# Performance work log

Measured on AMD Instinct MI355X. Metric: run time of the kernel, lower is better.

Reference implementation:

```python
import jax, jax.numpy as jnp
import numpy as np

N = 100_000      # nodes
E = 1_600_000    # edges
F_IN = 128       # n_features == conv_dim1..3
F_OUT = 256      # concat_dim
G = 2000         # number of graphs in the batch
EPS = 1e-5       # BatchNorm eps


def _xavier(k, shape):
    fan_in, fan_out = shape[-2], shape[-1]
    lim = float(np.sqrt(6.0 / (fan_in + fan_out)))
    return jax.random.uniform(k, shape, jnp.float32, -lim, lim)


def setup_inputs() -> dict:
    key = jax.random.key(0)
    ks = jax.random.split(key, 8)
    x = jax.random.normal(ks[0], (N, F_IN), jnp.float32)
    edge_index = jax.random.randint(ks[1], (2, E), 0, N, dtype=jnp.int64)
    batch = jnp.sort(jax.random.randint(ks[2], (N,), 0, G, dtype=jnp.int64))
    # layers 1..5: F_IN -> F_IN (stacked), layer 6: F_IN -> F_OUT
    Wi = _xavier(ks[3], (5, F_IN, F_IN))   # ARMA init_weight per layer
    Wr = _xavier(ks[4], (5, F_IN, F_IN))   # ARMA root_weight per layer
    b = jnp.zeros((5, F_IN), jnp.float32)  # ARMA bias per layer
    g = jnp.ones((5, F_IN), jnp.float32)   # BN gamma
    be = jnp.zeros((5, F_IN), jnp.float32) # BN beta
    Wi6 = _xavier(ks[5], (F_IN, F_OUT))
    Wr6 = _xavier(ks[6], (F_IN, F_OUT))
    b6 = jnp.zeros((F_OUT,), jnp.float32)
    g6 = jnp.ones((F_OUT,), jnp.float32)
    be6 = jnp.zeros((F_OUT,), jnp.float32)
    return dict(x=x, edge_index=edge_index, batch=batch, Wi=Wi, Wr=Wr, b=b,
                g=g, be=be, Wi6=Wi6, Wr6=Wr6, b6=b6, g6=g6, be6=be6)


def _arma(x, norm, row, col, Wi_l, Wr_l, b_l):
    # ARMAConv (num_stacks=1, num_layers=1, act=ReLU):
    #   out = ReLU( A_norm @ (x W_init) + x W_root + b )
    h = x @ Wi_l                                           # [N, F_out]
    msg = h[row] * norm[:, None]                           # gather + scale, [E, F_out]
    agg = jax.ops.segment_sum(msg, col, num_segments=N)    # scatter-add
    return jax.nn.relu(agg + x @ Wr_l + b_l)


def _bn(x, gamma, beta):
    # BatchNorm1d, training mode (biased batch variance)
    mu = x.mean(axis=0)
    var = x.var(axis=0)
    return gamma * (x - mu) * jax.lax.rsqrt(var + EPS) + beta


def reference(x, edge_index, batch, Wi, Wr, b, g, be, Wi6, Wr6, b6, g6, be6):
    row, col = edge_index[0], edge_index[1]
    # gcn_norm without self loops: D^-1/2 A D^-1/2 edge weights
    deg = jax.ops.segment_sum(jnp.ones((E,), x.dtype), col, num_segments=N)
    dinv = jnp.where(deg > 0, jax.lax.rsqrt(deg), 0.0)
    norm = dinv[row] * dinv[col]                           # [E]

    h = x
    for l in range(5):  # fixed small layer count
        h = _arma(h, norm, row, col, Wi[l], Wr[l], b[l])   # outer F.relu is idempotent
        h = _bn(h, g[l], be[l])
    h = _arma(h, norm, row, col, Wi6, Wr6, b6)
    h = _bn(h, g6, be6)
    # global_add_pool over graph ids; dropout = identity (deterministic baseline)
    out = jax.ops.segment_sum(h, batch, num_segments=G)    # [G, F_OUT]
    return out
```

## Files before the change

kernel.cpp:

```cpp
#include <hip/hip_runtime.h>

#define Nn 100000
#define NP 100001
#define Ee 1600000
#define Gg 2000
#define EPSf 1e-5f

typedef unsigned short ushort_t;
typedef __attribute__((ext_vector_type(8))) short short8;
typedef __attribute__((ext_vector_type(4))) float f32x4;
typedef __attribute__((ext_vector_type(4))) unsigned u32x4;

__device__ inline float bf2f(unsigned int u) {
    union { unsigned int i; float f; } v; v.i = u << 16; return v.f;
}
__device__ inline unsigned short f2bf(float f) {
    unsigned int x = __float_as_uint(f);
    unsigned int r = (x + 0x7fffu + ((x >> 16) & 1u)) >> 16;
    return (unsigned short)r;
}
__device__ inline int ldidx(const void* a, int i, int i64) {
    return i64 ? (int)((const long long*)a)[i] : ((const int*)a)[i];
}
__device__ inline float ldflt(const void* p, long long i, int f32) {
    return f32 ? ((const float*)p)[i] : bf2f(((const ushort_t*)p)[i]);
}


__global__ void k_flags(const void* gones, const void* ei, int* flags) {
    if (threadIdx.x == 0 && blockIdx.x == 0) {
        unsigned w = *(const unsigned*)gones;
        flags[0] = (w == 0x3F800000u) ? 1 : 0;
        const int* e = (const int*)ei;
        int nz = 0;
        for (int i = 0; i < 256; i++) nz |= e[2 * i + 1];
        flags[1] = nz ? 0 : 1;
    }
}


__global__ void k_hist(const void* __restrict__ ei, int* __restrict__ deg, const int* __restrict__ flags) {
    int i = blockIdx.x * 256 + threadIdx.x;
    if (i < Ee) {
        int c = ldidx(ei, Ee + i, flags[1]);
        atomicAdd(&deg[c], 1);
    }
}

__global__ void k_dinv(const int* __restrict__ deg, float* __restrict__ dinv) {
    int i = blockIdx.x * 256 + threadIdx.x;
    if (i < Nn) { int d = deg[i]; dinv[i] = d > 0 ? rsqrtf((float)d) : 0.f; }
}

__global__ void k_scan1(const int* __restrict__ deg, int* __restrict__ off, int* __restrict__ part) {
    __shared__ int sh[1024];
    int i = blockIdx.x * 1024 + threadIdx.x;
    int v = (i < Nn) ? ((deg[i] + 3) & ~3) : 0;
    sh[threadIdx.x] = v;
    __syncthreads();
    for (int ofs = 1; ofs < 1024; ofs <<= 1) {
        int t = 0;
        if ((int)threadIdx.x >= ofs) t = sh[threadIdx.x - ofs];
        __syncthreads();
        sh[threadIdx.x] += t;
        __syncthreads();
    }
    if (i < Nn) off[i] = sh[threadIdx.x] - v;
    if (threadIdx.x == 1023) part[blockIdx.x] = sh[1023];
}

__global__ void k_scan2(int* part, int nb) {
    if (threadIdx.x == 0 && blockIdx.x == 0) {
        int run = 0;
        for (int i = 0; i < nb; i++) { int t = part[i]; part[i] = run; run += t; }
        part[nb] = run;
    }
}

__global__ void k_scan3(int* __restrict__ off, const int* __restrict__ part, int* __restrict__ cursor) {
    int i = blockIdx.x * 256 + threadIdx.x;
    if (i < Nn) {
        int v = off[i] + part[i >> 10];
        off[i] = v;
        cursor[i] = v;
    }
    if (i == 0) off[Nn] = part[98];
}

__global__ void k_fillp(const void* __restrict__ ei, int* __restrict__ cursor,
                        int* __restrict__ srcS, const int* __restrict__ flags) {
    int range = blockIdx.x & 7;
    int e = (blockIdx.x >> 3) * 256 + threadIdx.x;
    if (e < Ee) {
        int i64 = flags[1];
        int c = ldidx(ei, Ee + e, i64);
        if (c >= range * 12500 && c < (range + 1) * 12500) {
            int r = ldidx(ei, e, i64);
            int p = atomicAdd(&cursor[c], 1);
            srcS[p] = r;
        }
    }
}

__global__ void k_pad(const int* __restrict__ cursor, const int* __restrict__ off,
                      int* __restrict__ srcS) {
    int i = blockIdx.x * 256 + threadIdx.x;
    if (i < Nn) {
        int e = off[i + 1];
        for (int p = cursor[i]; p < e; p++) srcS[p] = Nn;
    }
}

__global__ void k_zrow(ushort_t* __restrict__ Hi) {
    int t = threadIdx.x;
    int fc = t >> 4, j = t & 15;
    Hi[((size_t)fc * NP + Nn) * 16 + j] = 0;
}

__global__ void k_cvtp(const void* b, const void* b6, const void* g, const void* g6,
                       const void* be, const void* be6,
                       float* __restrict__ biasF, float* __restrict__ gF,
                       float* __restrict__ beF, const int* __restrict__ flags) {
    int i = blockIdx.x * 256 + threadIdx.x;
    if (i >= 2688) return;
    int grp = i / 896, r = i - grp * 896;
    int f32 = flags[0];
    const void* srcs[6] = { b, b6, g, g6, be, be6 };
    float* dsts[3] = { biasF, gF, beF };
    const void* s = (r < 640) ? srcs[grp * 2] : srcs[grp * 2 + 1];
    int idx = (r < 640) ? r : r - 640;
    dsts[grp][r] = ldflt(s, idx, f32);
}

__global__ void k_cvtx(const void* __restrict__ x, ushort_t* __restrict__ xq, const int* __restrict__ flags) {
    int node = blockIdx.x * 256 + threadIdx.x;
    int fc = blockIdx.y;
    if (node < Nn) {
        union { ushort_t u[16]; u32x4 v[2]; } t;
        if (flags[0]) {
            const float* p = (const float*)x + (size_t)node * 128 + fc * 16;
#pragma unroll
            for (int j = 0; j < 16; j++) t.u[j] = f2bf(p[j]);
        } else {
            const ushort_t* p = (const ushort_t*)x + (size_t)node * 128 + fc * 16;
#pragma unroll
            for (int j = 0; j < 16; j++) t.u[j] = p[j];
        }
        u32x4* d = (u32x4*)(xq + ((size_t)fc * Nn + node) * 16);
        d[0] = t.v[0]; d[1] = t.v[1];
    }
}

__global__ void k_pack(const void* __restrict__ Wi, const void* __restrict__ Wr,
                       const void* __restrict__ Wi6, const void* __restrict__ Wr6,
                       ushort_t* __restrict__ Bp, const int* __restrict__ flags) {
    int idx = blockIdx.x * 256 + threadIdx.x;
    if (idx >= 229376) return;
    int f32 = flags[0];
    if (idx < 163840) {
        int l = idx / 32768, rem = idx - l * 32768;
        int kg = rem / 2048, rem2 = rem - kg * 2048;
        int n = rem2 / 8, j = rem2 - n * 8;
        int k = kg * 8 + j;
        float v = (n < 128) ? ldflt(Wi, (l * 128 + k) * 128 + n, f32)
                            : ldflt(Wr, (l * 128 + k) * 128 + (n - 128), f32);
        Bp[idx] = f2bf(v);
    } else {
        int idx2 = idx - 163840;
        int kg = idx2 / 4096, rem2 = idx2 - kg * 4096;
        int n = rem2 / 8, j = rem2 - n * 8;
        int k = kg * 8 + j;
        float v = (n < 256) ? ldflt(Wi6, k * 256 + n, f32) : ldflt(Wr6, k * 256 + (n - 256), f32);
        Bp[idx] = f2bf(v);
    }
}

__global__ void k_fold(const ushort_t* __restrict__ Bp, const float* __restrict__ stat,
                       const float* __restrict__ gamma, const float* __restrict__ beta,
                       const float* __restrict__ bias,
                       ushort_t* __restrict__ Bp2, float* __restrict__ hcorr, int ncat) {
    __shared__ float red[128];
    int n = blockIdx.x, k = threadIdx.x;
    int fhalf = ncat >> 1;
    float mu = stat[k] * (1.f / Nn);
    float var = stat[128 + k] * (1.f / Nn) - mu * mu;
    float rs = rsqrtf(var + EPSf);
    float s = gamma[k] * rs;
    float h = beta[k] - s * mu;
    size_t idx = ((size_t)(k >> 3) * ncat + n) * 8 + (k & 7);
    float w = bf2f(Bp[idx]);
    Bp2[idx] = f2bf(w * s);
    red[k] = h * w;
    __syncthreads();
    for (int m = 64; m > 0; m >>= 1) { if (k < m) red[k] += red[k + m]; __syncthreads(); }
    if (k == 0) hcorr[n] = red[0] + (n >= fhalf ? bias[n - fhalf] : 0.f);
}

__global__ void k_h0(const float* __restrict__ bias, float* __restrict__ hc, int ncat) {
    int n = blockIdx.x * 256 + threadIdx.x;
    if (n < ncat) hc[n] = n >= (ncat >> 1) ? bias[n - (ncat >> 1)] : 0.f;
}


__global__ __launch_bounds__(256) void k_gemm(
        const ushort_t* __restrict__ Aq,
        const ushort_t* __restrict__ Bp, const float* __restrict__ hcorr,
        const float* __restrict__ dinv,
        ushort_t* __restrict__ Hi, ushort_t* __restrict__ yq, int ncat) {
    __shared__ ushort_t stage[32 * 264];
    const int tid = threadIdx.x, lane = tid & 63, wid = tid >> 6;
    const int q = lane >> 4, l15 = lane & 15;
    const int fhalf = ncat >> 1;
    const int colW = blockIdx.y * 256 + wid * 64;

    short8 bfr[4][4];
    float hc[4];
#pragma unroll
    for (int kk = 0; kk < 4; kk++) {
        int kg = kk * 4 + q;
#pragma unroll
        for (int ct = 0; ct < 4; ct++)
            bfr[kk][ct] = *(const short8*)(Bp + ((size_t)kg * ncat + colW + ct * 16 + l15) * 8);
    }
#pragma unroll
    for (int ct = 0; ct < 4; ct++) hc[ct] = hcorr[colW + ct * 16 + l15];

    for (int t = 0; t < 4; t++) {
        int row0 = (blockIdx.x * 4 + t) * 64;
        if (row0 >= Nn) break;

        f32x4 acc[4][4];
        f32x4 z; z.x = 0.f; z.y = 0.f; z.z = 0.f; z.w = 0.f;
#pragma unroll
        for (int rt = 0; rt < 4; rt++)
#pragma unroll
            for (int ct = 0; ct < 4; ct++) acc[rt][ct] = z;

#pragma unroll
        for (int kk = 0; kk < 4; kk++) {
            int kg = kk * 4 + q;
            const ushort_t* ap = Aq + (size_t)(kg >> 1) * Nn * 16 + (kg & 1) * 8;
            short8 af[4];
#pragma unroll
            for (int rt = 0; rt < 4; rt++) {
                int node = row0 + rt * 16 + l15;
                if (node >= Nn) node = Nn - 1;
                af[rt] = *(const short8*)(ap + (size_t)node * 16);
            }
#pragma unroll
            for (int rt = 0; rt < 4; rt++)
#pragma unroll
                for (int ct = 0; ct < 4; ct++)
                    acc[rt][ct] = __builtin_amdgcn_mfma_f32_16x16x32_bf16(af[rt], bfr[kk][ct], acc[rt][ct], 0, 0, 0);
        }

#pragma unroll
        for (int half = 0; half < 2; half++) {
            __syncthreads();
#pragma unroll
            for (int ct = 0; ct < 4; ct++) {
                int lcol = wid * 64 + ct * 16 + l15;
                bool isHi = (blockIdx.y * 256 + lcol) < fhalf;
#pragma unroll
                for (int rt2 = 0; rt2 < 2; rt2++) {
                    int rt = half * 2 + rt2;
#pragma unroll
                    for (int r = 0; r < 4; r++) {
                        int grow = row0 + rt * 16 + q * 4 + r;
                        int gr = grow < Nn ? grow : 0;
                        float v = acc[rt][ct][r] + hc[ct];
                        if (isHi) v *= dinv[gr];
                        stage[(rt2 * 16 + q * 4 + r) * 264 + lcol] = f2bf(v);
                    }
                }
            }
            __syncthreads();
            for (int chunk = tid; chunk < 512; chunk += 256) {
                int cg = chunk & 15, rl = chunk >> 4;
                int node = row0 + half * 32 + rl;
                if (node < Nn) {
                    int gc0 = blockIdx.y * 256 + cg * 16;
                    const u32x4* sp = (const u32x4*)&stage[rl * 264 + cg * 16];
                    u32x4 v0 = sp[0], v1 = sp[1];
                    ushort_t* dst = (gc0 < fhalf)
                        ? Hi + ((size_t)(gc0 >> 4) * NP + node) * 16
                        : yq + ((size_t)((gc0 - fhalf) >> 4) * Nn + node) * 16;
                    u32x4* dp = (u32x4*)dst;
                    dp[0] = v0; dp[1] = v1;
                }
            }
        }
    }
}


__global__ __launch_bounds__(256) void k_agg8(const int* __restrict__ off, const int* __restrict__ src,
                                              const float* __restrict__ dinv, const unsigned* __restrict__ Hi2,
                                              unsigned* __restrict__ yq, float* __restrict__ stat,
                                              int F, int fcbase) {
    const int tid = threadIdx.x;
    const int w = tid >> 6, lane = tid & 63;
    const int sub = lane >> 3, fl = lane & 7;
    const int fc = fcbase + (blockIdx.x & 7);
    const int T = blockIdx.x >> 3;
    const unsigned* __restrict__ base = Hi2 + (size_t)fc * (NP * 8) + fl;
    float st0 = 0.f, st1 = 0.f, st2 = 0.f, st3 = 0.f;

#pragma unroll
    for (int pass = 0; pass < 4; pass++) {
        int node = T * 128 + pass * 32 + w * 8 + sub;
        bool valid = node < Nn;
        int p0 = 0, p1 = 0;
        if (valid) { p0 = off[node]; p1 = off[node + 1]; }
        float a0 = 0.f, a1 = 0.f;
        int p = p0;
        for (; p + 15 < p1; p += 16) {
            int4 sa = *(const int4*)(src + p);
            int4 sb = *(const int4*)(src + p + 4);
            int4 sc = *(const int4*)(src + p + 8);
            int4 sd = *(const int4*)(src + p + 12);
            unsigned u0 = base[(unsigned)sa.x * 8u];
            unsigned u1 = base[(unsigned)sa.y * 8u];
            unsigned u2 = base[(unsigned)sa.z * 8u];
            unsigned u3 = base[(unsigned)sa.w * 8u];
            unsigned u4 = base[(unsigned)sb.x * 8u];
            unsigned u5 = base[(unsigned)sb.y * 8u];
            unsigned u6 = base[(unsigned)sb.z * 8u];
            unsigned u7 = base[(unsigned)sb.w * 8u];
            unsigned u8 = base[(unsigned)sc.x * 8u];
            unsigned u9 = base[(unsigned)sc.y * 8u];
            unsigned uA = base[(unsigned)sc.z * 8u];
            unsigned uB = base[(unsigned)sc.w * 8u];
            unsigned uC = base[(unsigned)sd.x * 8u];
            unsigned uD = base[(unsigned)sd.y * 8u];
            unsigned uE = base[(unsigned)sd.z * 8u];
            unsigned uF = base[(unsigned)sd.w * 8u];
            a0 += bf2f(u0 & 0xffffu); a1 += bf2f(u0 >> 16);
            a0 += bf2f(u1 & 0xffffu); a1 += bf2f(u1 >> 16);
            a0 += bf2f(u2 & 0xffffu); a1 += bf2f(u2 >> 16);
            a0 += bf2f(u3 & 0xffffu); a1 += bf2f(u3 >> 16);
            a0 += bf2f(u4 & 0xffffu); a1 += bf2f(u4 >> 16);
            a0 += bf2f(u5 & 0xffffu); a1 += bf2f(u5 >> 16);
            a0 += bf2f(u6 & 0xffffu); a1 += bf2f(u6 >> 16);
            a0 += bf2f(u7 & 0xffffu); a1 += bf2f(u7 >> 16);
            a0 += bf2f(u8 & 0xffffu); a1 += bf2f(u8 >> 16);
            a0 += bf2f(u9 & 0xffffu); a1 += bf2f(u9 >> 16);
            a0 += bf2f(uA & 0xffffu); a1 += bf2f(uA >> 16);
            a0 += bf2f(uB & 0xffffu); a1 += bf2f(uB >> 16);
            a0 += bf2f(uC & 0xffffu); a1 += bf2f(uC >> 16);
            a0 += bf2f(uD & 0xffffu); a1 += bf2f(uD >> 16);
            a0 += bf2f(uE & 0xffffu); a1 += bf2f(uE >> 16);
            a0 += bf2f(uF & 0xffffu); a1 += bf2f(uF >> 16);
        }
        for (; p + 7 < p1; p += 8) {
            int4 sa = *(const int4*)(src + p);
            int4 sb = *(const int4*)(src + p + 4);
            unsigned u0 = base[(unsigned)sa.x * 8u];
            unsigned u1 = base[(unsigned)sa.y * 8u];
            unsigned u2 = base[(unsigned)sa.z * 8u];
            unsigned u3 = base[(unsigned)sa.w * 8u];
            unsigned u4 = base[(unsigned)sb.x * 8u];
            unsigned u5 = base[(unsigned)sb.y * 8u];
            unsigned u6 = base[(unsigned)sb.z * 8u];
            unsigned u7 = base[(unsigned)sb.w * 8u];
            a0 += bf2f(u0 & 0xffffu); a1 += bf2f(u0 >> 16);
            a0 += bf2f(u1 & 0xffffu); a1 += bf2f(u1 >> 16);
            a0 += bf2f(u2 & 0xffffu); a1 += bf2f(u2 >> 16);
            a0 += bf2f(u3 & 0xffffu); a1 += bf2f(u3 >> 16);
            a0 += bf2f(u4 & 0xffffu); a1 += bf2f(u4 >> 16);
            a0 += bf2f(u5 & 0xffffu); a1 += bf2f(u5 >> 16);
            a0 += bf2f(u6 & 0xffffu); a1 += bf2f(u6 >> 16);
            a0 += bf2f(u7 & 0xffffu); a1 += bf2f(u7 >> 16);
        }
        if (p < p1) {
            int4 sa = *(const int4*)(src + p);
            unsigned u0 = base[(unsigned)sa.x * 8u];
            unsigned u1 = base[(unsigned)sa.y * 8u];
            unsigned u2 = base[(unsigned)sa.z * 8u];
            unsigned u3 = base[(unsigned)sa.w * 8u];
            a0 += bf2f(u0 & 0xffffu); a1 += bf2f(u0 >> 16);
            a0 += bf2f(u1 & 0xffffu); a1 += bf2f(u1 >> 16);
            a0 += bf2f(u2 & 0xffffu); a1 += bf2f(u2 >> 16);
            a0 += bf2f(u3 & 0xffffu); a1 += bf2f(u3 >> 16);
        }
        if (valid) {
            float dv = dinv[node];
            unsigned* yp = yq + ((size_t)fc * Nn + node) * 8 + fl;
            unsigned uv = *yp;
            float vx = fmaxf(bf2f(uv & 0xffffu) + dv * a0, 0.f);
            float vy = fmaxf(bf2f(uv >> 16) + dv * a1, 0.f);
            *yp = (unsigned)f2bf(vx) | ((unsigned)f2bf(vy) << 16);
            st0 += vx; st1 += vx * vx;
            st2 += vy; st3 += vy * vy;
        }
    }
#pragma unroll
    for (int m = 8; m <= 32; m <<= 1) {
        st0 += __shfl_xor(st0, m, 64);
        st1 += __shfl_xor(st1, m, 64);
        st2 += __shfl_xor(st2, m, 64);
        st3 += __shfl_xor(st3, m, 64);
    }
    __shared__ float red[4][8][4];
    if (sub == 0) {
        red[w][fl][0] = st0; red[w][fl][1] = st1;
        red[w][fl][2] = st2; red[w][fl][3] = st3;
    }
    __syncthreads();
    if (tid < 32) {
        int rfl = tid >> 2, k = tid & 3;
        float s = red[0][rfl][k] + red[1][rfl][k] + red[2][rfl][k] + red[3][rfl][k];
        int f = fc * 16 + rfl * 2 + (k >> 1);
        atomicAdd(&stat[(k & 1) * F + f], s);
    }
}


__device__ inline int lb(const void* a, int n, int key, int i64) {
    int lo = 0, hi = n;
    while (lo < hi) { int mid = (lo + hi) >> 1; if (ldidx(a, mid, i64) < key) lo = mid + 1; else hi = mid; }
    return lo;
}

__global__ void k_pool(const ushort_t* __restrict__ y6q, const float* __restrict__ stat,
                       const float* __restrict__ g6, const float* __restrict__ be6,
                       const void* __restrict__ batch, void* __restrict__ out,
                       const int* __restrict__ flags) {
    int g = blockIdx.x;
    int f = threadIdx.x;
    int i64 = flags[1];
    int start = lb(batch, Nn, g, i64);
    int end = lb(batch, Nn, g + 1, i64);
    const ushort_t* yp = y6q + (size_t)(f >> 4) * Nn * 16 + (f & 15);
    float s = 0.f;
    for (int n = start; n < end; n++) s += bf2f(yp[(size_t)n * 16]);
    int cnt = end - start;
    float mu = stat[f] * (1.f / Nn);
    float var = stat[256 + f] * (1.f / Nn) - mu * mu;
    float rs = rsqrtf(var + EPSf);
    float val = g6[f] * rs * (s - (float)cnt * mu) + (float)cnt * be6[f];
    if (flags[0]) ((float*)out)[(size_t)g * 256 + f] = val;
    else          ((ushort_t*)out)[(size_t)g * 256 + f] = f2bf(val);
}


extern "C" void kernel_launch(void* const* d_in, const int* in_sizes, int n_in,
                              void* d_out, int out_size, void* d_ws, size_t ws_size,
                              hipStream_t stream) {
    const void* x    = d_in[0];
    const void* ei   = d_in[1];
    const void* batch= d_in[2];
    const void* Wi   = d_in[3];
    const void* Wr   = d_in[4];
    const void* b    = d_in[5];
    const void* g    = d_in[6];
    const void* be   = d_in[7];
    const void* Wi6  = d_in[8];
    const void* Wr6  = d_in[9];
    const void* b6   = d_in[10];
    const void* g6   = d_in[11];
    const void* be6  = d_in[12];

    char* p = (char*)d_ws;
    auto alloc = [&](size_t bytes) { char* r = p; p += (bytes + 511) & ~(size_t)511; return r; };
    ushort_t* HiB  = (ushort_t*)alloc((size_t)NP * 256 * 2);
    ushort_t* xq   = (ushort_t*)alloc((size_t)Nn * 128 * 2);
    ushort_t* yAq  = (ushort_t*)alloc((size_t)Nn * 128 * 2);
    ushort_t* yBq  = (ushort_t*)alloc((size_t)Nn * 128 * 2);
    ushort_t* y6q  = (ushort_t*)alloc((size_t)Nn * 256 * 2);
    int* srcS      = (int*)alloc(((size_t)Ee + 4 * Nn + 64) * 4);
    int* off       = (int*)alloc((size_t)(Nn + 1) * 4);
    int* cursor    = (int*)alloc((size_t)Nn * 4);
    int* deg       = (int*)alloc((size_t)Nn * 4);
    float* dinv    = (float*)alloc((size_t)Nn * 4);
    int* part      = (int*)alloc(128 * 4);
    float* statsA  = (float*)alloc(6 * 512 * 4);
    ushort_t* Bp   = (ushort_t*)alloc(229376 * 2);
    ushort_t* Bp2  = (ushort_t*)alloc(65536 * 2);
    float* hcorrA  = (float*)alloc(512 * 4);
    int* flags     = (int*)alloc(2 * 4);
    float* biasF   = (float*)alloc(896 * 4);
    float* gF      = (float*)alloc(896 * 4);
    float* beF     = (float*)alloc(896 * 4);
    const unsigned* Hi2 = (const unsigned*)HiB;

    const int AGG_GRID = 782 * 8;
    const int GEMM_GRID = 391;

    k_flags<<<1, 64, 0, stream>>>(g, ei, flags);
    k_cvtp<<<11, 256, 0, stream>>>(b, b6, g, g6, be, be6, biasF, gF, beF, flags);

    hipMemsetAsync(deg, 0, (size_t)Nn * 4, stream);
    hipMemsetAsync(statsA, 0, 6 * 512 * 4, stream);
    k_hist<<<6250, 256, 0, stream>>>(ei, deg, flags);
    k_dinv<<<391, 256, 0, stream>>>(deg, dinv);
    k_scan1<<<98, 1024, 0, stream>>>(deg, off, part);
    k_scan2<<<1, 64, 0, stream>>>(part, 98);
    k_scan3<<<391, 256, 0, stream>>>(off, part, cursor);
    k_fillp<<<50000, 256, 0, stream>>>(ei, cursor, srcS, flags);
    k_pad<<<391, 256, 0, stream>>>(cursor, off, srcS);
    k_zrow<<<1, 256, 0, stream>>>(HiB);
    k_pack<<<896, 256, 0, stream>>>(Wi, Wr, Wi6, Wr6, Bp, flags);
    k_cvtx<<<dim3(391, 8), 256, 0, stream>>>(x, xq, flags);
    k_h0<<<1, 256, 0, stream>>>(biasF, hcorrA, 256);

    k_gemm<<<dim3(GEMM_GRID, 1), 256, 0, stream>>>(xq, Bp, hcorrA, dinv, HiB, yAq, 256);
    k_agg8<<<AGG_GRID, 256, 0, stream>>>(off, srcS, dinv, Hi2, (unsigned*)yAq, statsA, 128, 0);
    k_fold<<<256, 128, 0, stream>>>(Bp + 32768, statsA, gF, beF, biasF + 128, Bp2, hcorrA, 256);

    k_gemm<<<dim3(GEMM_GRID, 1), 256, 0, stream>>>(yAq, Bp2, hcorrA, dinv, HiB, yBq, 256);
    k_agg8<<<AGG_GRID, 256, 0, stream>>>(off, srcS, dinv, Hi2, (unsigned*)yBq, statsA + 512, 128, 0);
    k_fold<<<256, 128, 0, stream>>>(Bp + 65536, statsA + 512, gF + 128, beF + 128, biasF + 256, Bp2, hcorrA, 256);

    k_gemm<<<dim3(GEMM_GRID, 1), 256, 0, stream>>>(yBq, Bp2, hcorrA, dinv, HiB, yAq, 256);
    k_agg8<<<AGG_GRID, 256, 0, stream>>>(off, srcS, dinv, Hi2, (unsigned*)yAq, statsA + 1024, 128, 0);
    k_fold<<<256, 128, 0, stream>>>(Bp + 98304, statsA + 1024, gF + 256, beF + 256, biasF + 384, Bp2, hcorrA, 256);

    k_gemm<<<dim3(GEMM_GRID, 1), 256, 0, stream>>>(yAq, Bp2, hcorrA, dinv, HiB, yBq, 256);
    k_agg8<<<AGG_GRID, 256, 0, stream>>>(off, srcS, dinv, Hi2, (unsigned*)yBq, statsA + 1536, 128, 0);
    k_fold<<<256, 128, 0, stream>>>(Bp + 131072, statsA + 1536, gF + 384, beF + 384, biasF + 512, Bp2, hcorrA, 256);

    k_gemm<<<dim3(GEMM_GRID, 1), 256, 0, stream>>>(yBq, Bp2, hcorrA, dinv, HiB, yAq, 256);
    k_agg8<<<AGG_GRID, 256, 0, stream>>>(off, srcS, dinv, Hi2, (unsigned*)yAq, statsA + 2048, 128, 0);
    k_fold<<<512, 128, 0, stream>>>(Bp + 163840, statsA + 2048, gF + 512, beF + 512, biasF + 640, Bp2, hcorrA, 512);

    k_gemm<<<dim3(GEMM_GRID, 2), 256, 0, stream>>>(yAq, Bp2, hcorrA, dinv, HiB, y6q, 512);
    k_agg8<<<AGG_GRID, 256, 0, stream>>>(off, srcS, dinv, Hi2, (unsigned*)y6q, statsA + 2560, 256, 0);
    k_agg8<<<AGG_GRID, 256, 0, stream>>>(off, srcS, dinv, Hi2, (unsigned*)y6q, statsA + 2560, 256, 8);
    k_pool<<<Gg, 256, 0, stream>>>(y6q, statsA + 2560, gF + 640, beF + 640, batch, d_out, flags);
}
```

Before: 1.244 ms.

## Sort nodes by degree bucket for aggregation and shrink GEMM tiles per block

Adds a counting sort of nodes into degree buckets (histogram, prefix, scatter) so the aggregation kernel processes nodes of similar degree together through a permutation, reducing lane divergence and load imbalance within waves. The GEMM kernel now processes one 64-row tile per block instead of four, with a correspondingly larger grid, to increase parallelism. The cost is three extra setup kernels, an extra indirection per node in aggregation that scatters the output writes, and the loss of per-block reuse of loaded B fragments across tiles.

```diff
diff --git a/kernel.cpp b/kernel.cpp
--- a/kernel.cpp
+++ b/kernel.cpp
@@ -115,6 +115,31 @@
     int t = threadIdx.x;
     int fc = t >> 4, j = t & 15;
     Hi[((size_t)fc * NP + Nn) * 16 + j] = 0;
+}
+
+
+__global__ void k_bh(const int* __restrict__ deg, int* __restrict__ bh) {
+    int i = blockIdx.x * 256 + threadIdx.x;
+    if (i < Nn) {
+        int b = (deg[i] + 3) >> 2; if (b > 255) b = 255;
+        atomicAdd(&bh[b], 1);
+    }
+}
+
+__global__ void k_bp(const int* __restrict__ bh, int* __restrict__ bc) {
+    if (threadIdx.x == 0 && blockIdx.x == 0) {
+        int run = 0;
+        for (int i = 0; i < 256; i++) { bc[i] = run; run += bh[i]; }
+    }
+}
+
+__global__ void k_bs(const int* __restrict__ deg, int* __restrict__ bc, int* __restrict__ perm) {
+    int i = blockIdx.x * 256 + threadIdx.x;
+    if (i < Nn) {
+        int b = (deg[i] + 3) >> 2; if (b > 255) b = 255;
+        int p = atomicAdd(&bc[b], 1);
+        perm[p] = i;
+    }
 }
 
 __global__ void k_cvtp(const void* b, const void* b6, const void* g, const void* g6,
@@ -212,6 +237,7 @@
     const int q = lane >> 4, l15 = lane & 15;
     const int fhalf = ncat >> 1;
     const int colW = blockIdx.y * 256 + wid * 64;
+    const int row0 = blockIdx.x * 64;
 
     short8 bfr[4][4];
     float hc[4];
@@ -225,69 +251,64 @@
 #pragma unroll
     for (int ct = 0; ct < 4; ct++) hc[ct] = hcorr[colW + ct * 16 + l15];
 
-    for (int t = 0; t < 4; t++) {
-        int row0 = (blockIdx.x * 4 + t) * 64;
-        if (row0 >= Nn) break;
-
-        f32x4 acc[4][4];
-        f32x4 z; z.x = 0.f; z.y = 0.f; z.z = 0.f; z.w = 0.f;
+    f32x4 acc[4][4];
+    f32x4 z; z.x = 0.f; z.y = 0.f; z.z = 0.f; z.w = 0.f;
+#pragma unroll
+    for (int rt = 0; rt < 4; rt++)
+#pragma unroll
+        for (int ct = 0; ct < 4; ct++) acc[rt][ct] = z;
+
+#pragma unroll
+    for (int kk = 0; kk < 4; kk++) {
+        int kg = kk * 4 + q;
+        const ushort_t* ap = Aq + (size_t)(kg >> 1) * Nn * 16 + (kg & 1) * 8;
+        short8 af[4];
+#pragma unroll
+        for (int rt = 0; rt < 4; rt++) {
+            int node = row0 + rt * 16 + l15;
+            if (node >= Nn) node = Nn - 1;
+            af[rt] = *(const short8*)(ap + (size_t)node * 16);
+        }
 #pragma unroll
         for (int rt = 0; rt < 4; rt++)
 #pragma unroll
-            for (int ct = 0; ct < 4; ct++) acc[rt][ct] = z;
-
-#pragma unroll
-        for (int kk = 0; kk < 4; kk++) {
-            int kg = kk * 4 + q;
-            const ushort_t* ap = Aq + (size_t)(kg >> 1) * Nn * 16 + (kg & 1) * 8;
-            short8 af[4];
-#pragma unroll
-            for (int rt = 0; rt < 4; rt++) {
-                int node = row0 + rt * 16 + l15;
-                if (node >= Nn) node = Nn - 1;
-                af[rt] = *(const short8*)(ap + (size_t)node * 16);
-            }
-#pragma unroll
-            for (int rt = 0; rt < 4; rt++)
-#pragma unroll
-                for (int ct = 0; ct < 4; ct++)
-                    acc[rt][ct] = __builtin_amdgcn_mfma_f32_16x16x32_bf16(af[rt], bfr[kk][ct], acc[rt][ct], 0, 0, 0);
-        }
-
-#pragma unroll
-        for (int half = 0; half < 2; half++) {
-            __syncthreads();
-#pragma unroll
-            for (int ct = 0; ct < 4; ct++) {
-                int lcol = wid * 64 + ct * 16 + l15;
-                bool isHi = (blockIdx.y * 256 + lcol) < fhalf;
-#pragma unroll
-                for (int rt2 = 0; rt2 < 2; rt2++) {
-                    int rt = half * 2 + rt2;
-#pragma unroll
-                    for (int r = 0; r < 4; r++) {
-                        int grow = row0 + rt * 16 + q * 4 + r;
-                        int gr = grow < Nn ? grow : 0;
-                        float v = acc[rt][ct][r] + hc[ct];
-                        if (isHi) v *= dinv[gr];
-                        stage[(rt2 * 16 + q * 4 + r) * 264 + lcol] = f2bf(v);
-                    }
+            for (int ct = 0; ct < 4; ct++)
+                acc[rt][ct] = __builtin_amdgcn_mfma_f32_16x16x32_bf16(af[rt], bfr[kk][ct], acc[rt][ct], 0, 0, 0);
+    }
+
+#pragma unroll
+    for (int half = 0; half < 2; half++) {
+        __syncthreads();
+#pragma unroll
+        for (int ct = 0; ct < 4; ct++) {
+            int lcol = wid * 64 + ct * 16 + l15;
+            bool isHi = (blockIdx.y * 256 + lcol) < fhalf;
+#pragma unroll
+            for (int rt2 = 0; rt2 < 2; rt2++) {
+                int rt = half * 2 + rt2;
+#pragma unroll
+                for (int r = 0; r < 4; r++) {
+                    int grow = row0 + rt * 16 + q * 4 + r;
+                    int gr = grow < Nn ? grow : 0;
+                    float v = acc[rt][ct][r] + hc[ct];
+                    if (isHi) v *= dinv[gr];
+                    stage[(rt2 * 16 + q * 4 + r) * 264 + lcol] = f2bf(v);
                 }
             }
-            __syncthreads();
-            for (int chunk = tid; chunk < 512; chunk += 256) {
-                int cg = chunk & 15, rl = chunk >> 4;
-                int node = row0 + half * 32 + rl;
-                if (node < Nn) {
-                    int gc0 = blockIdx.y * 256 + cg * 16;
-                    const u32x4* sp = (const u32x4*)&stage[rl * 264 + cg * 16];
-                    u32x4 v0 = sp[0], v1 = sp[1];
-                    ushort_t* dst = (gc0 < fhalf)
-                        ? Hi + ((size_t)(gc0 >> 4) * NP + node) * 16
-                        : yq + ((size_t)((gc0 - fhalf) >> 4) * Nn + node) * 16;
-                    u32x4* dp = (u32x4*)dst;
-                    dp[0] = v0; dp[1] = v1;
-                }
+        }
+        __syncthreads();
+        for (int chunk = tid; chunk < 512; chunk += 256) {
+            int cg = chunk & 15, rl = chunk >> 4;
+            int node = row0 + half * 32 + rl;
+            if (node < Nn) {
+                int gc0 = blockIdx.y * 256 + cg * 16;
+                const u32x4* sp = (const u32x4*)&stage[rl * 264 + cg * 16];
+                u32x4 v0 = sp[0], v1 = sp[1];
+                ushort_t* dst = (gc0 < fhalf)
+                    ? Hi + ((size_t)(gc0 >> 4) * NP + node) * 16
+                    : yq + ((size_t)((gc0 - fhalf) >> 4) * Nn + node) * 16;
+                u32x4* dp = (u32x4*)dst;
+                dp[0] = v0; dp[1] = v1;
             }
         }
     }
@@ -295,6 +316,7 @@
 
 
 __global__ __launch_bounds__(256) void k_agg8(const int* __restrict__ off, const int* __restrict__ src,
+                                              const int* __restrict__ perm,
                                               const float* __restrict__ dinv, const unsigned* __restrict__ Hi2,
                                               unsigned* __restrict__ yq, float* __restrict__ stat,
                                               int F, int fcbase) {
@@ -308,10 +330,14 @@
 
 #pragma unroll
     for (int pass = 0; pass < 4; pass++) {
-        int node = T * 128 + pass * 32 + w * 8 + sub;
-        bool valid = node < Nn;
+        int sIdx = T * 128 + pass * 32 + w * 8 + sub;
+        bool valid = sIdx < Nn;
+        int node = 0;
         int p0 = 0, p1 = 0;
-        if (valid) { p0 = off[node]; p1 = off[node + 1]; }
+        if (valid) {
+            node = perm[sIdx];
+            p0 = off[node]; p1 = off[node + 1];
+        }
         float a0 = 0.f, a1 = 0.f;
         int p = p0;
         for (; p + 15 < p1; p += 16) {
@@ -474,6 +500,9 @@
     int* deg       = (int*)alloc((size_t)Nn * 4);
     float* dinv    = (float*)alloc((size_t)Nn * 4);
     int* part      = (int*)alloc(128 * 4);
+    int* perm      = (int*)alloc((size_t)Nn * 4);
+    int* bh        = (int*)alloc(256 * 4);
+    int* bc        = (int*)alloc(256 * 4);
     float* statsA  = (float*)alloc(6 * 512 * 4);
     ushort_t* Bp   = (ushort_t*)alloc(229376 * 2);
     ushort_t* Bp2  = (ushort_t*)alloc(65536 * 2);
@@ -485,12 +514,13 @@
     const unsigned* Hi2 = (const unsigned*)HiB;
 
     const int AGG_GRID = 782 * 8;
-    const int GEMM_GRID = 391;
+    const int GEMM_GRID = 1563;
 
     k_flags<<<1, 64, 0, stream>>>(g, ei, flags);
     k_cvtp<<<11, 256, 0, stream>>>(b, b6, g, g6, be, be6, biasF, gF, beF, flags);
 
     hipMemsetAsync(deg, 0, (size_t)Nn * 4, stream);
+    hipMemsetAsync(bh, 0, 256 * 4, stream);
     hipMemsetAsync(statsA, 0, 6 * 512 * 4, stream);
     k_hist<<<6250, 256, 0, stream>>>(ei, deg, flags);
     k_dinv<<<391, 256, 0, stream>>>(deg, dinv);
@@ -500,32 +530,35 @@
     k_fillp<<<50000, 256, 0, stream>>>(ei, cursor, srcS, flags);
     k_pad<<<391, 256, 0, stream>>>(cursor, off, srcS);
     k_zrow<<<1, 256, 0, stream>>>(HiB);
+    k_bh<<<391, 256, 0, stream>>>(deg, bh);
+    k_bp<<<1, 64, 0, stream>>>(bh, bc);
+    k_bs<<<391, 256, 0, stream>>>(deg, bc, perm);
     k_pack<<<896, 256, 0, stream>>>(Wi, Wr, Wi6, Wr6, Bp, flags);
     k_cvtx<<<dim3(391, 8), 256, 0, stream>>>(x, xq, flags);
     k_h0<<<1, 256, 0, stream>>>(biasF, hcorrA, 256);
 
     k_gemm<<<dim3(GEMM_GRID, 1), 256, 0, stream>>>(xq, Bp, hcorrA, dinv, HiB, yAq, 256);
-    k_agg8<<<AGG_GRID, 256, 0, stream>>>(off, srcS, dinv, Hi2, (unsigned*)yAq, statsA, 128, 0);
+    k_agg8<<<AGG_GRID, 256, 0, stream>>>(off, srcS, perm, dinv, Hi2, (unsigned*)yAq, statsA, 128, 0);
     k_fold<<<256, 128, 0, stream>>>(Bp + 32768, statsA, gF, beF, biasF + 128, Bp2, hcorrA, 256);
 
     k_gemm<<<dim3(GEMM_GRID, 1), 256, 0, stream>>>(yAq, Bp2, hcorrA, dinv, HiB, yBq, 256);
-    k_agg8<<<AGG_GRID, 256, 0, stream>>>(off, srcS, dinv, Hi2, (unsigned*)yBq, statsA + 512, 128, 0);
+    k_agg8<<<AGG_GRID, 256, 0, stream>>>(off, srcS, perm, dinv, Hi2, (unsigned*)yBq, statsA + 512, 128, 0);
     k_fold<<<256, 128, 0, stream>>>(Bp + 65536, statsA + 512, gF + 128, beF + 128, biasF + 256, Bp2, hcorrA, 256);
 
     k_gemm<<<dim3(GEMM_GRID, 1), 256, 0, stream>>>(yBq, Bp2, hcorrA, dinv, HiB, yAq, 256);
-    k_agg8<<<AGG_GRID, 256, 0, stream>>>(off, srcS, dinv, Hi2, (unsigned*)yAq, statsA + 1024, 128, 0);
+    k_agg8<<<AGG_GRID, 256, 0, stream>>>(off, srcS, perm, dinv, Hi2, (unsigned*)yAq, statsA + 1024, 128, 0);
     k_fold<<<256, 128, 0, stream>>>(Bp + 98304, statsA + 1024, gF + 256, beF + 256, biasF + 384, Bp2, hcorrA, 256);
 
     k_gemm<<<dim3(GEMM_GRID, 1), 256, 0, stream>>>(yAq, Bp2, hcorrA, dinv, HiB, yBq, 256);
-    k_agg8<<<AGG_GRID, 256, 0, stream>>>(off, srcS, dinv, Hi2, (unsigned*)yBq, statsA + 1536, 128, 0);
+    k_agg8<<<AGG_GRID, 256, 0, stream>>>(off, srcS, perm, dinv, Hi2, (unsigned*)yBq, statsA + 1536, 128, 0);
     k_fold<<<256, 128, 0, stream>>>(Bp + 131072, statsA + 1536, gF + 384, beF + 384, biasF + 512, Bp2, hcorrA, 256);
 
     k_gemm<<<dim3(GEMM_GRID, 1), 256, 0, stream>>>(yBq, Bp2, hcorrA, dinv, HiB, yAq, 256);
-    k_agg8<<<AGG_GRID, 256, 0, stream>>>(off, srcS, dinv, Hi2, (unsigned*)yAq, statsA + 2048, 128, 0);
+    k_agg8<<<AGG_GRID, 256, 0, stream>>>(off, srcS, perm, dinv, Hi2, (unsigned*)yAq, statsA + 2048, 128, 0);
     k_fold<<<512, 128, 0, stream>>>(Bp + 163840, statsA + 2048, gF + 512, beF + 512, biasF + 640, Bp2, hcorrA, 512);
 
     k_gemm<<<dim3(GEMM_GRID, 2), 256, 0, stream>>>(yAq, Bp2, hcorrA, dinv, HiB, y6q, 512);
-    k_agg8<<<AGG_GRID, 256, 0, stream>>>(off, srcS, dinv, Hi2, (unsigned*)y6q, statsA + 2560, 256, 0);
-    k_agg8<<<AGG_GRID, 256, 0, stream>>>(off, srcS, dinv, Hi2, (unsigned*)y6q, statsA + 2560, 256, 8);
+    k_agg8<<<AGG_GRID, 256, 0, stream>>>(off, srcS, perm, dinv, Hi2, (unsigned*)y6q, statsA + 2560, 256, 0);
+    k_agg8<<<AGG_GRID, 256, 0, stream>>>(off, srcS, perm, dinv, Hi2, (unsigned*)y6q, statsA + 2560, 256, 8);
     k_pool<<<Gg, 256, 0, stream>>>(y6q, statsA + 2560, gF + 640, beF + 640, batch, d_out, flags);
 }
```

Result: slower. 2.468 ms (+98.4%).
